# Optimization experiments

Hardware: AMD Instinct MI355X
Metric: run time of the kernel (lower is better)

The kernel has to match this reference:

```python
import jax, jax.numpy as jnp
import numpy as np

HEADS = 4
DIM_HEAD = 32
SCALE = 10.0
EPS = 1e-12


def setup_inputs() -> dict:
    key = jax.random.key(0)
    k1, k2, k3 = jax.random.split(key, 3)
    B, D, H, W, C = 2, 8, 16, 32, 128
    dim = HEADS * DIM_HEAD  # 128
    x = jax.random.normal(k1, (B, D, H, W, C), dtype=jnp.float32)
    # 1x1x1 convs are matmuls over the channel dim
    w_qkv = jax.random.normal(k2, (C, 3 * dim), dtype=jnp.float32) * (1.0 / np.sqrt(C))
    w_out = jax.random.normal(k3, (dim, C), dtype=jnp.float32) * (1.0 / np.sqrt(dim))
    b_out = jnp.zeros((C,), dtype=jnp.float32)
    return {"x": x, "w_qkv": w_qkv, "w_out": w_out, "b_out": b_out}


def reference(x, w_qkv, w_out, b_out):
    B, D, H, W, C = x.shape
    N = D * H * W
    dim = HEADS * DIM_HEAD
    xf = x.reshape(B, N, C)
    qkv = xf @ w_qkv                                   # [B, N, 3*dim]
    q, k, v = jnp.split(qkv, 3, axis=-1)
    def to_heads(t):
        return t.reshape(B, N, HEADS, DIM_HEAD)        # [B, N, h, d]
    q, k, v = to_heads(q), to_heads(k), to_heads(v)
    # L2-normalize q and k along head dim (cosine attention)
    q = q / jnp.clip(jnp.linalg.norm(q, axis=-1, keepdims=True), EPS)
    k = k / jnp.clip(jnp.linalg.norm(k, axis=-1, keepdims=True), EPS)
    sim = jnp.einsum('bihd,bjhd->bhij', q, k) * SCALE  # [B, h, N, N]
    attn = jax.nn.softmax(sim, axis=-1)
    out = jnp.einsum('bhij,bjhd->bihd', attn, v)       # [B, N, h, d]
    out = out.reshape(B, N, dim)
    out = out @ w_out + b_out                          # [B, N, C]
    return out.reshape(B, D, H, W, C)
```

## Files before the change

### kernel.cpp

```cpp
#include <hip/hip_runtime.h>
#include <math.h>

#define HEADS   4
#define DH      32
#define NB      4096
#define BATCH   2
#define C_IN    128
#define QKV_COLS 384
#define TOTROWS 8192
#define ATT_EPS 1e-12f
#define C1      14.42695040888963f
#define QROWS   8
#define OROWS   8

typedef __attribute__((ext_vector_type(16))) float f32x16;
typedef _Float16 f16x8 __attribute__((ext_vector_type(8)));
typedef __fp16 fp16x2 __attribute__((ext_vector_type(2)));
typedef unsigned short u16;

__device__ __forceinline__ u16 f16b(float a) {
  union { _Float16 h; u16 u; } t; t.h = (_Float16)a; return t.u;
}
__device__ __forceinline__ unsigned pkf16rtn(float a, float b) {
  return (unsigned)f16b(a) | ((unsigned)f16b(b) << 16);
}
union Uh2 { fp16x2 h; unsigned u; };
__device__ __forceinline__ unsigned pkf16(float a, float b) {
  Uh2 t; t.h = __builtin_amdgcn_cvt_pkrtz(a, b); return t.u;
}
union U8h { unsigned u[4]; f16x8 h8; };
__device__ __forceinline__ f16x8 mk8h(unsigned a, unsigned b, unsigned c, unsigned d) {
  U8h t; t.u[0] = a; t.u[1] = b; t.u[2] = c; t.u[3] = d; return t.h8;
}
__device__ __forceinline__ void pl32swap(unsigned& a, unsigned& b) {
  asm("v_permlane32_swap_b32 %0, %1" : "+v"(a), "+v"(b));
}

__global__ __launch_bounds__(384) void qkv_kernel(
    const float* __restrict__ x, const float* __restrict__ w,
    float* __restrict__ Qs, u16* __restrict__ K16, u16* __restrict__ VT16) {
  const int tid = threadIdx.x;
  const int r0  = blockIdx.x * QROWS;

  float4 a4[QROWS];
#pragma unroll
  for (int r = 0; r < QROWS; ++r) a4[r] = make_float4(0.f, 0.f, 0.f, 0.f);

  for (int c4 = 0; c4 < 32; ++c4) {
    const float wv0 = w[(c4 * 4 + 0) * QKV_COLS + tid];
    const float wv1 = w[(c4 * 4 + 1) * QKV_COLS + tid];
    const float wv2 = w[(c4 * 4 + 2) * QKV_COLS + tid];
    const float wv3 = w[(c4 * 4 + 3) * QKV_COLS + tid];
#pragma unroll
    for (int r = 0; r < QROWS; ++r) {
      const float* xr = x + (size_t)(r0 + r) * C_IN + c4 * 4;
      a4[r].x = fmaf(xr[0], wv0, a4[r].x);
      a4[r].y = fmaf(xr[1], wv1, a4[r].y);
      a4[r].z = fmaf(xr[2], wv2, a4[r].z);
      a4[r].w = fmaf(xr[3], wv3, a4[r].w);
    }
  }

  float acc[QROWS];
#pragma unroll
  for (int r = 0; r < QROWS; ++r)
    acc[r] = (a4[r].x + a4[r].y) + (a4[r].z + a4[r].w);

  const int part = tid >> 7;
  if (part < 2) {
#pragma unroll
    for (int r = 0; r < QROWS; ++r) {
      float s = acc[r] * acc[r];
      s += __shfl_xor(s, 1, 32);
      s += __shfl_xor(s, 2, 32);
      s += __shfl_xor(s, 4, 32);
      s += __shfl_xor(s, 8, 32);
      s += __shfl_xor(s, 16, 32);
      acc[r] *= 1.0f / fmaxf(sqrtf(s), ATT_EPS);
    }
  }

  const int h = (tid >> 5) & 3, d = tid & 31;
  const int b = r0 >> 12, n0 = r0 & (NB - 1);
  const int bh = b * HEADS + h;
  if (part == 0) {
    float* dst = Qs + ((size_t)bh * NB + n0) * DH + d;
#pragma unroll
    for (int r = 0; r < QROWS; ++r) dst[(size_t)r * DH] = acc[r] * C1;
  } else if (part == 1) {
    const size_t kb = ((size_t)bh * NB + n0) * DH + d;
#pragma unroll
    for (int r = 0; r < QROWS; ++r) K16[kb + (size_t)r * DH] = f16b(acc[r]);
  } else {
    const size_t vb = ((size_t)bh * DH + d) * NB + n0;
#pragma unroll
    for (int r = 0; r < QROWS; r += 4) {
      uint2 hv;
      hv.x = pkf16rtn(acc[r + 0], acc[r + 1]);
      hv.y = pkf16rtn(acc[r + 2], acc[r + 3]);
      *(uint2*)(VT16 + vb + r) = hv;
    }
  }
}

__global__ __launch_bounds__(512, 4) void attn_kernel(
    const float* __restrict__ Qs, const u16* __restrict__ K16,
    const u16* __restrict__ VT16, float* __restrict__ AO) {
  __shared__ float mrg[2 * 3 * 32 * 33 + 2 * 3 * 32];
  float* const mO = mrg;
  float* const mL = mrg + 2 * 3 * 32 * 33;

  const int tid  = threadIdx.x;
  const int lane = tid & 63;
  const int w    = tid >> 6;
  const int su   = w & 3;
  const int u    = w >> 2;
  const int q    = lane & 31;
  const int hi   = lane >> 5;
  const int bh   = blockIdx.x & 7;
  const int qp   = blockIdx.x >> 3;

  const int nrow = qp * 64 + u * 32 + q;
  const float* qrow = Qs + ((size_t)bh * NB + nrow) * DH;
  f16x8 fq16[2];
#pragma unroll
  for (int sl = 0; sl < 2; ++sl) {
    const int d0 = sl * 16 + hi * 8;
    const float4 a = *(const float4*)(qrow + d0);
    const float4 b = *(const float4*)(qrow + d0 + 4);
    fq16[sl] = mk8h(pkf16rtn(a.x, a.y), pkf16rtn(a.z, a.w),
                    pkf16rtn(b.x, b.y), pkf16rtn(b.z, b.w));
  }

  const u16* kp = K16 + (size_t)bh * NB * DH + (size_t)(su * 1024 + q) * DH + hi * 8;
  const u16* vp = VT16 + (size_t)bh * DH * NB + (size_t)q * NB + su * 1024 + hi * 8;

  f32x16 oa, zz;
#pragma unroll
  for (int r = 0; r < 16; ++r) { oa[r] = 0.f; zz[r] = 0.f; }
  float lrun = 0.f;

#pragma unroll 2
  for (int t = 0; t < 32; ++t) {
    const f16x8 fk0 = *(const f16x8*)(kp);
    const f16x8 fk1 = *(const f16x8*)(kp + 16);
    const f16x8 fv0 = *(const f16x8*)(vp);
    const f16x8 fv1 = *(const f16x8*)(vp + 16);
    kp += 32 * DH;
    vp += 32;

    f32x16 sa;
    __builtin_amdgcn_s_setprio(1);
    sa = __builtin_amdgcn_mfma_f32_32x32x16_f16(fk0, fq16[0], zz, 0, 0, 0);
    sa = __builtin_amdgcn_mfma_f32_32x32x16_f16(fk1, fq16[1], sa, 0, 0, 0);
    __builtin_amdgcn_s_setprio(0);

    float e[16], lsum = 0.f;
#pragma unroll
    for (int r = 0; r < 16; ++r) {
      e[r] = __builtin_amdgcn_exp2f(sa[r]);
      lsum += e[r];
    }
    lrun += lsum;

    __builtin_amdgcn_s_setprio(1);
    {
      unsigned x0 = pkf16(e[0], e[1]), x1 = pkf16(e[2], e[3]);
      unsigned y0 = pkf16(e[4], e[5]), y1 = pkf16(e[6], e[7]);
      pl32swap(x0, y0);
      pl32swap(x1, y1);
      oa = __builtin_amdgcn_mfma_f32_32x32x16_f16(fv0, mk8h(x0, x1, y0, y1),
                                                  oa, 0, 0, 0);
      unsigned z0 = pkf16(e[8], e[9]),  z1 = pkf16(e[10], e[11]);
      unsigned t0 = pkf16(e[12], e[13]), t1 = pkf16(e[14], e[15]);
      pl32swap(z0, t0);
      pl32swap(z1, t1);
      oa = __builtin_amdgcn_mfma_f32_32x32x16_f16(fv1, mk8h(z0, z1, t0, t1),
                                                  oa, 0, 0, 0);
    }
    __builtin_amdgcn_s_setprio(0);
  }

  const float Lfull = lrun + __shfl_xor(lrun, 32);
  if (su != 0) {
    const int sidx = (u * 3 + (su - 1)) * 32 + q;
    if (hi == 0) mL[sidx] = Lfull;
#pragma unroll
    for (int r = 0; r < 16; ++r) {
      const int d = (r & 3) + 8 * (r >> 2) + 4 * hi;
      mO[sidx * 33 + d] = oa[r];
    }
  }
  __syncthreads();
  if (su == 0) {
    float Lt = Lfull;
#pragma unroll
    for (int s = 0; s < 3; ++s) Lt += mL[(u * 3 + s) * 32 + q];
    const float inv = 1.0f / Lt;
    const int b = bh >> 2, h = bh & 3;
    float* dst = AO + ((size_t)(b * NB + nrow)) * 128 + h * DH;
#pragma unroll
    for (int r = 0; r < 16; ++r) {
      const int d = (r & 3) + 8 * (r >> 2) + 4 * hi;
      float v = oa[r];
#pragma unroll
      for (int s = 0; s < 3; ++s) v += mO[((u * 3 + s) * 32 + q) * 33 + d];
      dst[d] = v * inv;
    }
  }
}

__global__ __launch_bounds__(128) void outproj_kernel(
    const float* __restrict__ AO, const float* __restrict__ w,
    const float* __restrict__ bias, float* __restrict__ out) {
  const int tid = threadIdx.x;
  const int r0  = blockIdx.x * OROWS;

  float4 a4[OROWS];
#pragma unroll
  for (int r = 0; r < OROWS; ++r) a4[r] = make_float4(0.f, 0.f, 0.f, 0.f);

  for (int c4 = 0; c4 < 32; ++c4) {
    const float wv0 = w[(c4 * 4 + 0) * 128 + tid];
    const float wv1 = w[(c4 * 4 + 1) * 128 + tid];
    const float wv2 = w[(c4 * 4 + 2) * 128 + tid];
    const float wv3 = w[(c4 * 4 + 3) * 128 + tid];
#pragma unroll
    for (int r = 0; r < OROWS; ++r) {
      const float* xr = AO + (size_t)(r0 + r) * 128 + c4 * 4;
      a4[r].x = fmaf(xr[0], wv0, a4[r].x);
      a4[r].y = fmaf(xr[1], wv1, a4[r].y);
      a4[r].z = fmaf(xr[2], wv2, a4[r].z);
      a4[r].w = fmaf(xr[3], wv3, a4[r].w);
    }
  }

  __syncthreads();

  const float bv = bias[tid];
#pragma unroll
  for (int r = 0; r < OROWS; ++r) {
    const float acc = (a4[r].x + a4[r].y) + (a4[r].z + a4[r].w);
    out[(size_t)(r0 + r) * 128 + tid] = acc + bv;
  }
}

extern "C" void kernel_launch(void* const* d_in, const int* in_sizes, int n_in,
                              void* d_out, int out_size, void* d_ws, size_t ws_size,
                              hipStream_t stream) {
  (void)in_sizes; (void)n_in; (void)out_size; (void)ws_size;
  const float* x     = (const float*)d_in[0];
  const float* w_qkv = (const float*)d_in[1];
  const float* w_out = (const float*)d_in[2];
  const float* b_out = (const float*)d_in[3];
  float* out = (float*)d_out;

  float* ws = (float*)d_ws;
  float* Qs = ws;
  u16* K16  = (u16*)(ws + 1048576);
  u16* VT16 = K16 + 1048576;
  float* AO = out;

  qkv_kernel<<<TOTROWS / QROWS, 384, 0, stream>>>(x, w_qkv, Qs, K16, VT16);
  attn_kernel<<<512, 512, 0, stream>>>(Qs, K16, VT16, AO);
  outproj_kernel<<<TOTROWS / OROWS, 128, 0, stream>>>(AO, w_out, b_out, out);
}
```

Measured before the change: 81.87 us.

## Stage K tiles through LDS asynchronously and split keys eight ways per block

```diff
diff --git a/kernel.cpp b/kernel.cpp
--- a/kernel.cpp
+++ b/kernel.cpp
@@ -35,6 +35,10 @@
 __device__ __forceinline__ void pl32swap(unsigned& a, unsigned& b) {
   asm("v_permlane32_swap_b32 %0, %1" : "+v"(a), "+v"(b));
 }
+#define GL16(gp, lp)                                                        \
+  __builtin_amdgcn_global_load_lds(                                         \
+      (const __attribute__((address_space(1))) void*)(gp),                  \
+      (__attribute__((address_space(3))) void*)(lp), 16, 0, 0)
 
 __global__ __launch_bounds__(384) void qkv_kernel(
     const float* __restrict__ x, const float* __restrict__ w,
@@ -103,24 +107,20 @@
   }
 }
 
-__global__ __launch_bounds__(512, 4) void attn_kernel(
+__global__ __launch_bounds__(512, 8) void attn_kernel(
     const float* __restrict__ Qs, const u16* __restrict__ K16,
     const u16* __restrict__ VT16, float* __restrict__ AO) {
-  __shared__ float mrg[2 * 3 * 32 * 33 + 2 * 3 * 32];
-  float* const mO = mrg;
-  float* const mL = mrg + 2 * 3 * 32 * 33;
+  __shared__ __align__(16) char sbuf[2][8][2048];
 
   const int tid  = threadIdx.x;
   const int lane = tid & 63;
-  const int w    = tid >> 6;
-  const int su   = w & 3;
-  const int u    = w >> 2;
+  const int su   = tid >> 6;
   const int q    = lane & 31;
   const int hi   = lane >> 5;
   const int bh   = blockIdx.x & 7;
   const int qp   = blockIdx.x >> 3;
 
-  const int nrow = qp * 64 + u * 32 + q;
+  const int nrow = qp * 32 + q;
   const float* qrow = Qs + ((size_t)bh * NB + nrow) * DH;
   f16x8 fq16[2];
 #pragma unroll
@@ -132,27 +132,60 @@
                     pkf16rtn(b.x, b.y), pkf16rtn(b.z, b.w));
   }
 
-  const u16* kp = K16 + (size_t)bh * NB * DH + (size_t)(su * 1024 + q) * DH + hi * 8;
-  const u16* vp = VT16 + (size_t)bh * DH * NB + (size_t)q * NB + su * 1024 + hi * 8;
+  const u16* gp[2]; int ldso[2];
+#pragma unroll
+  for (int it = 0; it < 2; ++it) {
+    const int idx  = tid + it * 512;
+    const int sp   = idx >> 7;
+    const int s    = idx & 127;
+    const int rtt  = s >> 2;
+    const int ps   = s & 3;
+    const int slot = ((ps ^ ((rtt >> 1) & 3)) << 3);
+    gp[it]  = K16 + (size_t)bh * NB * DH + (size_t)(sp * 512 + rtt) * DH + slot;
+    ldso[it] = idx * 16;
+  }
+  char* const sb = (char*)sbuf;
+  auto stage = [&](int buf) {
+#pragma unroll
+    for (int it = 0; it < 2; ++it) {
+      GL16(gp[it], sb + buf * 16384 + ldso[it]);
+      gp[it] += 32 * DH;
+    }
+  };
+
+  const u16* vp = VT16 + (size_t)bh * DH * NB + (size_t)q * NB + su * 512 + hi * 8;
+
+  const int swq = (q >> 1) & 3;
+  int koff[2];
+#pragma unroll
+  for (int i = 0; i < 2; ++i) koff[i] = q * 64 + (((i * 2 + hi) ^ swq) << 4);
 
   f32x16 oa, zz;
 #pragma unroll
   for (int r = 0; r < 16; ++r) { oa[r] = 0.f; zz[r] = 0.f; }
   float lrun = 0.f;
 
-#pragma unroll 2
-  for (int t = 0; t < 32; ++t) {
-    const f16x8 fk0 = *(const f16x8*)(kp);
-    const f16x8 fk1 = *(const f16x8*)(kp + 16);
+  stage(0);
+  __syncthreads();
+
+  for (int t = 0; t < 16; ++t) {
+    const int cur = t & 1;
+    if (t < 15) stage(cur ^ 1);
+
     const f16x8 fv0 = *(const f16x8*)(vp);
     const f16x8 fv1 = *(const f16x8*)(vp + 16);
-    kp += 32 * DH;
     vp += 32;
+
+    const char* ck = sb + cur * 16384 + su * 2048;
 
     f32x16 sa;
     __builtin_amdgcn_s_setprio(1);
-    sa = __builtin_amdgcn_mfma_f32_32x32x16_f16(fk0, fq16[0], zz, 0, 0, 0);
-    sa = __builtin_amdgcn_mfma_f32_32x32x16_f16(fk1, fq16[1], sa, 0, 0, 0);
+    {
+      const f16x8 fk0 = *(const f16x8*)(ck + koff[0]);
+      const f16x8 fk1 = *(const f16x8*)(ck + koff[1]);
+      sa = __builtin_amdgcn_mfma_f32_32x32x16_f16(fk0, fq16[0], zz, 0, 0, 0);
+      sa = __builtin_amdgcn_mfma_f32_32x32x16_f16(fk1, fq16[1], sa, 0, 0, 0);
+    }
     __builtin_amdgcn_s_setprio(0);
 
     float e[16], lsum = 0.f;
@@ -171,7 +204,7 @@
       pl32swap(x1, y1);
       oa = __builtin_amdgcn_mfma_f32_32x32x16_f16(fv0, mk8h(x0, x1, y0, y1),
                                                   oa, 0, 0, 0);
-      unsigned z0 = pkf16(e[8], e[9]),  z1 = pkf16(e[10], e[11]);
+      unsigned z0 = pkf16(e[8], e[9]),   z1 = pkf16(e[10], e[11]);
       unsigned t0 = pkf16(e[12], e[13]), t1 = pkf16(e[14], e[15]);
       pl32swap(z0, t0);
       pl32swap(z1, t1);
@@ -179,11 +212,14 @@
                                                   oa, 0, 0, 0);
     }
     __builtin_amdgcn_s_setprio(0);
-  }
-
+    __syncthreads();
+  }
+
+  float* const mO = (float*)sbuf;
+  float* const mL = mO + 7 * 32 * 33;
   const float Lfull = lrun + __shfl_xor(lrun, 32);
   if (su != 0) {
-    const int sidx = (u * 3 + (su - 1)) * 32 + q;
+    const int sidx = (su - 1) * 32 + q;
     if (hi == 0) mL[sidx] = Lfull;
 #pragma unroll
     for (int r = 0; r < 16; ++r) {
@@ -195,7 +231,7 @@
   if (su == 0) {
     float Lt = Lfull;
 #pragma unroll
-    for (int s = 0; s < 3; ++s) Lt += mL[(u * 3 + s) * 32 + q];
+    for (int s = 0; s < 7; ++s) Lt += mL[s * 32 + q];
     const float inv = 1.0f / Lt;
     const int b = bh >> 2, h = bh & 3;
     float* dst = AO + ((size_t)(b * NB + nrow)) * 128 + h * DH;
@@ -204,7 +240,7 @@
       const int d = (r & 3) + 8 * (r >> 2) + 4 * hi;
       float v = oa[r];
 #pragma unroll
-      for (int s = 0; s < 3; ++s) v += mO[((u * 3 + s) * 32 + q) * 33 + d];
+      for (int s = 0; s < 7; ++s) v += mO[(s * 32 + q) * 33 + d];
       dst[d] = v * inv;
     }
   }
@@ -262,6 +298,6 @@
   float* AO = out;
 
   qkv_kernel<<<TOTROWS / QROWS, 384, 0, stream>>>(x, w_qkv, Qs, K16, VT16);
-  attn_kernel<<<512, 512, 0, stream>>>(Qs, K16, VT16, AO);
+  attn_kernel<<<1024, 512, 0, stream>>>(Qs, K16, VT16, AO);
   outproj_kernel<<<TOTROWS / OROWS, 128, 0, stream>>>(AO, w_out, b_out, out);
 }
```

After: 84.76 us. 3.5% more time.
